# Performance work log

Measured on AMD Instinct MI355X. Metric: run time of the kernel, lower is better.

The kernel has to match this reference:

```python
import jax, jax.numpy as jnp
import numpy as np

L = 4      # number of Verifier layers in the linked list
D = 1536   # constraint matrix dimension


def setup_inputs() -> dict:
    key = jax.random.key(0)
    ks = jax.random.split(key, 6)
    scale = 0.02  # keep chained matmul magnitudes sane
    lb = jax.random.normal(ks[0], (1, D), jnp.float32)
    ub = lb + jax.random.uniform(ks[1], (1, D), jnp.float32)  # ensure lb <= ub
    lcs = scale * jax.random.normal(ks[2], (L, D, D), jnp.float32)
    ucs = lcs + scale * jax.random.uniform(ks[3], (L, D, D), jnp.float32)
    lc_bias = jax.random.normal(ks[4], (L, D), jnp.float32)
    uc_bias = lc_bias + jax.random.uniform(ks[5], (L, D), jnp.float32)
    return {"lb": lb, "ub": ub, "lcs": lcs, "ucs": ucs,
            "lc_bias": lc_bias, "uc_bias": uc_bias}


def reference(lb, ub, lcs, ucs, lc_bias, uc_bias):
    pos = lambda x: jnp.maximum(x, 0.0)
    neg = lambda x: jnp.minimum(x, 0.0)
    n_layers = lcs.shape[0]

    # Layer 0 forward: its backsubstitution returns these bounds unchanged
    # (prev is None), and all later backsubs terminate on these stored bounds.
    lb0 = lb @ pos(lcs[0]).T + ub @ neg(lcs[0]).T + lc_bias[0]
    ub0 = ub @ pos(ucs[0]).T + lb @ neg(ucs[0]).T + uc_bias[0]
    cur_lb, cur_ub = lb0, ub0

    for k in range(1, n_layers):
        # backsubstitution from layer k: start with transposed constraint
        C_lc, C_uc = lcs[k].T, ucs[k].T           # [D, D]
        C_lcb, C_ucb = lc_bias[k], uc_bias[k]     # [D]
        # recurse through layers k-1 .. 0, combining constraints
        for j in range(k - 1, -1, -1):
            pU, nU = pos(C_uc), neg(C_uc)
            pL, nL = pos(C_lc), neg(C_lc)
            new_ucb = uc_bias[j] @ pU + lc_bias[j] @ nU + C_ucb
            new_uc = ucs[j].T @ pU + lcs[j].T @ nU
            new_lcb = lc_bias[j] @ pL + uc_bias[j] @ nL + C_lcb
            new_lc = lcs[j].T @ pL + ucs[j].T @ nL
            C_lc, C_uc, C_lcb, C_ucb = new_lc, new_uc, new_lcb, new_ucb
        # apply combined constraint to layer-0 stored bounds
        cur_lb = lb0 @ pos(C_lc) + ub0 @ neg(C_lc) + C_lcb
        cur_ub = ub0 @ pos(C_uc) + lb0 @ neg(C_uc) + C_ucb

    return cur_lb, cur_ub
```

## Files before the change

### kernel.cpp

```cpp
#include <hip/hip_runtime.h>

#define D 1536
#define BT 96
#define BK 64
#define NT (D / BK)
#define TT 64
#define TILE_E (BT * BK)
#define BUF_E (3 * TILE_E)

typedef unsigned short u16;
typedef short bf16x8 __attribute__((ext_vector_type(8)));
typedef float f32x4 __attribute__((ext_vector_type(4)));

static __device__ __forceinline__ u16 f2bf(float f) {
    unsigned u; __builtin_memcpy(&u, &f, 4);
    unsigned r = (u + 0x7FFFu + ((u >> 16) & 1u)) >> 16;
    return (u16)r;
}
static __device__ __forceinline__ float bf2f(u16 s) {
    unsigned u = ((unsigned)s) << 16;
    float f; __builtin_memcpy(&f, &u, 4); return f;
}

#define GLDS(g, s) __builtin_amdgcn_global_load_lds( \
    (const __attribute__((address_space(1))) void*)(g), \
    (__attribute__((address_space(3))) void*)(s), 16, 0, 0)

#define MFMA16(a, b, c) __builtin_amdgcn_mfma_f32_16x16x32_bf16(a, b, c, 0, 0, 0)

__global__ __launch_bounds__(256) void prep_k(
    const float* __restrict__ lcs, const float* __restrict__ ucs,
    u16* __restrict__ BsT, u16* __restrict__ BdT,
    u16* __restrict__ Ga, u16* __restrict__ Gc)
{
    const int z = blockIdx.z;
    const int r0 = blockIdx.y * TT, c0 = blockIdx.x * TT;
    const int tid = threadIdx.x;

    if (z == 3) {
#pragma unroll
        for (int m = 0; m < 2; ++m) {
            const float* src = (m ? lcs : ucs) + (size_t)3 * D * D;
            u16* dst = m ? Gc : Ga;
#pragma unroll
            for (int i = 0; i < 2; ++i) {
                int r = (tid >> 3) + i * 32, cc = (tid & 7) * 8;
                const float* p = src + (size_t)(r0 + r) * D + c0 + cc;
                f32x4 x0 = *(const f32x4*)p;
                f32x4 x1 = *(const f32x4*)(p + 4);
                bf16x8 y;
#pragma unroll
                for (int e = 0; e < 4; ++e) { y[e] = (short)f2bf(x0[e]); y[e + 4] = (short)f2bf(x1[e]); }
                *(bf16x8*)(dst + (size_t)(r0 + r) * D + c0 + cc) = y;
            }
        }
        return;
    }

    __shared__ u16 ts[TT][TT + 8];
    __shared__ u16 td[TT][TT + 8];
    const float* srcl = lcs + (size_t)z * D * D;
    const float* srcu = ucs + (size_t)z * D * D;
#pragma unroll
    for (int i = 0; i < 2; ++i) {
        int c = tid + i * 256; int r = c >> 3, v = c & 7;
        size_t off = (size_t)(r0 + r) * D + c0 + v * 8;
        f32x4 l0 = *(const f32x4*)(srcl + off);
        f32x4 l1 = *(const f32x4*)(srcl + off + 4);
        f32x4 u0 = *(const f32x4*)(srcu + off);
        f32x4 u1 = *(const f32x4*)(srcu + off + 4);
        bf16x8 ys, yd;
#pragma unroll
        for (int e = 0; e < 4; ++e) {
            ys[e]     = (short)f2bf((u0[e] + l0[e]) * 0.5f);
            yd[e]     = (short)f2bf((u0[e] - l0[e]) * 0.5f);
            ys[e + 4] = (short)f2bf((u1[e] + l1[e]) * 0.5f);
            yd[e + 4] = (short)f2bf((u1[e] - l1[e]) * 0.5f);
        }
        *(bf16x8*)&ts[r][v * 8] = ys;
        *(bf16x8*)&td[r][v * 8] = yd;
    }
    __syncthreads();
#pragma unroll
    for (int i = 0; i < 2; ++i) {
        int c = tid + i * 256; int rr = c >> 3, v = c & 7;
        bf16x8 xs, xd;
#pragma unroll
        for (int e = 0; e < 8; ++e) { xs[e] = (short)ts[v * 8 + e][rr]; xd[e] = (short)td[v * 8 + e][rr]; }
        size_t off = (size_t)z * D * D + (size_t)(c0 + rr) * D + r0 + v * 8;
        *(bf16x8*)(BsT + off) = xs;
        *(bf16x8*)(BdT + off) = xd;
    }
}

__global__ __launch_bounds__(256) void vec_k(
    const float* __restrict__ lb, const float* __restrict__ ub,
    const float* __restrict__ lcs, const float* __restrict__ ucs,
    const float* __restrict__ lcb, const float* __restrict__ ucb,
    float* __restrict__ lb0, float* __restrict__ ub0,
    float* __restrict__ cb_uc, float* __restrict__ cb_lc)
{
    const int tt = blockIdx.x * 4 + (threadIdx.x >> 6);
    const int lane = threadIdx.x & 63;
    const int which = tt / D;
    const int row_n = tt - which * D;

    const float* row; const float* vp; const float* vn;
    if (which == 0)      { row = lcs + (size_t)row_n * D;               vp = lb;           vn = ub; }
    else if (which == 1) { row = ucs + (size_t)row_n * D;               vp = ub;           vn = lb; }
    else if (which == 2) { row = ucs + (size_t)(3 * (size_t)D * D) + (size_t)row_n * D; vp = ucb + 2 * D; vn = lcb + 2 * D; }
    else                 { row = lcs + (size_t)(3 * (size_t)D * D) + (size_t)row_n * D; vp = lcb + 2 * D; vn = ucb + 2 * D; }

    float s = 0.f;
    for (int c2 = 0; c2 < D / 256; ++c2) {
        int base = (c2 * 64 + lane) * 4;
        f32x4 g = *(const f32x4*)(row + base);
        f32x4 p = *(const f32x4*)(vp + base);
        f32x4 m = *(const f32x4*)(vn + base);
#pragma unroll
        for (int e = 0; e < 4; ++e) s += g[e] * (g[e] > 0.f ? p[e] : m[e]);
    }
#pragma unroll
    for (int o = 32; o; o >>= 1) s += __shfl_down(s, o);
    if (lane == 0) {
        if (which == 0)      lb0[row_n] = s + lcb[row_n];
        else if (which == 1) ub0[row_n] = s + ucb[row_n];
        else if (which == 2) cb_uc[row_n] = s + ucb[3 * D + row_n];
        else                 cb_lc[row_n] = s + lcb[3 * D + row_n];
    }
}

__global__ __launch_bounds__(256, 2) void gemm_step(
    const u16* __restrict__ Guc, const u16* __restrict__ Glc,
    const u16* __restrict__ Bs, const u16* __restrict__ Bd,
    u16* __restrict__ outU, u16* __restrict__ outL,
    const float* __restrict__ ucbN, const float* __restrict__ lcbN,
    float* __restrict__ cb_uc, float* __restrict__ cb_lc)
{
    __shared__ u16 smem[2 * BUF_E];
    const int wg  = blockIdx.x + 16 * blockIdx.y + 256 * blockIdx.z;
    const int xcd = wg & 7, idx = wg >> 3;
    const int chain = xcd >> 2;
    const int bx = (xcd & 1) * 8 + (idx & 7);
    const int by = ((xcd >> 1) & 1) * 8 + (idx >> 3);

    const u16* A = chain ? Glc : Guc;
    u16* out = chain ? outL : outU;
    const unsigned sgn = chain ? 0x80008000u : 0u;
    const int r0 = by * BT, c0 = bx * BT;
    const int tid = threadIdx.x, lane = tid & 63, wid = tid >> 6;
    const int mb = (wid >> 1) * 48, nb = (wid & 1) * 48;
    const int lrow = lane & 15, lk = lane >> 4;

    f32x4 acc[3][3] = {};

#define STAGE(kt, sbuf) do { \
    _Pragma("unroll") for (int i_ = 0; i_ < 9; ++i_) { \
        const int idx_ = (i_ % 3) * 256 + tid; \
        const int row_ = idx_ >> 3; \
        const int kcg_ = (tid & 7) ^ (row_ & 7); \
        const u16* base_ = (i_ < 3) ? (A + (size_t)(r0 + row_) * D) \
                        : ((i_ < 6) ? (Bs + (size_t)(c0 + row_) * D) \
                                    : (Bd + (size_t)(c0 + row_) * D)); \
        GLDS(base_ + (kt) + kcg_ * 8, (char*)(sbuf) + (i_ * 256 + wid * 64) * 16); \
    } } while (0)

    int offA[3], offBs[3], offBd[3];
#pragma unroll
    for (int mi = 0; mi < 3; ++mi) {
        int row = mb + mi * 16 + lrow;
        offA[mi] = row * BK + (lk ^ (row & 7)) * 8;
    }
#pragma unroll
    for (int ni = 0; ni < 3; ++ni) {
        int row = nb + ni * 16 + lrow;
        offBs[ni] = TILE_E + row * BK;
        offBd[ni] = 2 * TILE_E + row * BK;
    }

    STAGE(0, smem);
    STAGE(BK, smem + BUF_E);

#pragma unroll 1
    for (int t = 0; t < NT; ++t) {
        if (t < NT - 1) { asm volatile("s_waitcnt vmcnt(9)" ::: "memory"); }
        else            { asm volatile("s_waitcnt vmcnt(0)" ::: "memory"); }
        __builtin_amdgcn_sched_barrier(0);
        __builtin_amdgcn_s_barrier();

        const u16* sb = smem + (t & 1) * BUF_E;
#pragma unroll
        for (int ks = 0; ks < 2; ++ks) {
            const int slot = ks * 4;
            bf16x8 a[3], x[3];
#pragma unroll
            for (int mi = 0; mi < 3; ++mi) {
                int row = mb + mi * 16 + lrow;
                a[mi] = *(const bf16x8*)(sb + row * BK + ((slot + lk) ^ (row & 7)) * 8);
                union { bf16x8 v; unsigned u[4]; } ti, to;
                ti.v = a[mi];
#pragma unroll
                for (int q = 0; q < 4; ++q) to.u[q] = (ti.u[q] & 0x7FFF7FFFu) ^ sgn;
                x[mi] = to.v;
            }
#pragma unroll
            for (int ni = 0; ni < 3; ++ni) {
                int row = nb + ni * 16 + lrow;
                int o = row * BK + ((slot + lk) ^ (row & 7)) * 8;
                bf16x8 bs = *(const bf16x8*)(sb + TILE_E + o);
                bf16x8 bd = *(const bf16x8*)(sb + 2 * TILE_E + o);
#pragma unroll
                for (int mi = 0; mi < 3; ++mi) {
                    acc[mi][ni] = MFMA16(a[mi], bs, acc[mi][ni]);
                    acc[mi][ni] = MFMA16(x[mi], bd, acc[mi][ni]);
                }
            }
        }
        __builtin_amdgcn_s_barrier();
        if (t + 2 < NT)
            STAGE((t + 2) * BK, smem + (t & 1) * BUF_E);
    }

    if (ucbN) {
        const float* pb_ = chain ? lcbN : ucbN;
        const float* nb_ = chain ? ucbN : lcbN;
        float* cb = chain ? cb_lc : cb_uc;
        float pbv[3], nbv[3];
#pragma unroll
        for (int ni = 0; ni < 3; ++ni) {
            int c = c0 + nb + ni * 16 + lrow;
            pbv[ni] = pb_[c]; nbv[ni] = nb_[c];
        }
#pragma unroll
        for (int mi = 0; mi < 3; ++mi)
#pragma unroll
            for (int q = 0; q < 4; ++q) {
                float s = 0.f;
#pragma unroll
                for (int ni = 0; ni < 3; ++ni) {
                    float g = acc[mi][ni][q];
                    s += g * (g > 0.f ? pbv[ni] : nbv[ni]);
                }
                s += __shfl_xor(s, 1); s += __shfl_xor(s, 2);
                s += __shfl_xor(s, 4); s += __shfl_xor(s, 8);
                if (lrow == 0)
                    atomicAdd(&cb[r0 + mb + mi * 16 + lk * 4 + q], s);
            }
    }

#pragma unroll
    for (int mi = 0; mi < 3; ++mi)
#pragma unroll
        for (int ni = 0; ni < 3; ++ni) {
            int c = c0 + nb + ni * 16 + lrow;
            int rbase = r0 + mb + mi * 16 + lk * 4;
#pragma unroll
            for (int q = 0; q < 4; ++q)
                out[(size_t)(rbase + q) * D + c] = f2bf(acc[mi][ni][q]);
        }
#undef STAGE
}

__global__ __launch_bounds__(256) void final_k(
    const u16* __restrict__ Guc, const u16* __restrict__ Glc,
    const float* __restrict__ cb_uc, const float* __restrict__ cb_lc,
    const float* __restrict__ lb0, const float* __restrict__ ub0,
    float* __restrict__ out)
{
    const int gw = blockIdx.x * 4 + (threadIdx.x >> 6);
    const int lane = threadIdx.x & 63;
    const int which = gw >= D;
    const int n = which ? gw - D : gw;
    const u16* row = (which ? Guc : Glc) + (size_t)n * D;
    const float* vp = which ? ub0 : lb0;
    const float* vn = which ? lb0 : ub0;
    float s = 0.f;
    for (int c2 = 0; c2 < D / 512; ++c2) {
        int base = (c2 * 64 + lane) * 8;
        bf16x8 g8 = *(const bf16x8*)(row + base);
        f32x4 p0 = *(const f32x4*)(vp + base);
        f32x4 p1 = *(const f32x4*)(vp + base + 4);
        f32x4 n0 = *(const f32x4*)(vn + base);
        f32x4 n1 = *(const f32x4*)(vn + base + 4);
#pragma unroll
        for (int e = 0; e < 8; ++e) {
            float g = bf2f((u16)g8[e]);
            float pv = e < 4 ? p0[e] : p1[e - 4];
            float nv = e < 4 ? n0[e] : n1[e - 4];
            s += g * (g > 0.f ? pv : nv);
        }
    }
#pragma unroll
    for (int o = 32; o; o >>= 1) s += __shfl_down(s, o);
    if (lane == 0) {
        float b = (which ? cb_uc : cb_lc)[n];
        out[which * D + n] = s + b;
    }
}

extern "C" void kernel_launch(void* const* d_in, const int* in_sizes, int n_in,
                              void* d_out, int out_size, void* d_ws, size_t ws_size,
                              hipStream_t stream) {
    const float* lb  = (const float*)d_in[0];
    const float* ub  = (const float*)d_in[1];
    const float* lcs = (const float*)d_in[2];
    const float* ucs = (const float*)d_in[3];
    const float* lcb = (const float*)d_in[4];
    const float* ucb = (const float*)d_in[5];
    float* out = (float*)d_out;

    const size_t DD = (size_t)D * D;
    u16* ws   = (u16*)d_ws;
    u16* BsT = ws;
    u16* BdT = BsT + 3 * DD;
    u16* Ga = BdT + 3 * DD;
    u16* Gb = Ga + DD;
    u16* Gc = Gb + DD;
    u16* Gd = Gc + DD;
    float* fbuf  = (float*)(Gd + DD);
    float* lb0   = fbuf;
    float* ub0   = fbuf + D;
    float* cb_uc = fbuf + 2 * D;
    float* cb_lc = fbuf + 3 * D;

    prep_k<<<dim3(D / TT, D / TT, 4), 256, 0, stream>>>(lcs, ucs, BsT, BdT, Ga, Gc);
    vec_k<<<dim3(4 * D / 4), 256, 0, stream>>>(lb, ub, lcs, ucs, lcb, ucb, lb0, ub0, cb_uc, cb_lc);

    u16* curU = Ga; u16* curL = Gc;
    u16* altU = Gb; u16* altL = Gd;
    for (int j = 2; j >= 0; --j) {
        const float* ucbN = (j > 0) ? (ucb + (size_t)(j - 1) * D) : nullptr;
        const float* lcbN = (j > 0) ? (lcb + (size_t)(j - 1) * D) : nullptr;
        gemm_step<<<dim3(16, 16, 2), 256, 0, stream>>>(
            curU, curL, BsT + (size_t)j * DD, BdT + (size_t)j * DD, altU, altL,
            ucbN, lcbN, cb_uc, cb_lc);
        u16* t;
        t = curU; curU = altU; altU = t;
        t = curL; curL = altL; altL = t;
    }
    final_k<<<dim3(2 * D / 4), 256, 0, stream>>>(curU, curL, cb_uc, cb_lc, lb0, ub0, out);
}
```

Baseline: 129.1 us.

## Use per-wave private LDS staging to drop workgroup barriers in GEMM step

The shared 96x64 double-buffered tile, loaded cooperatively and guarded by two workgroup barriers per k-step, is replaced with per-wave private buffers. Each wave loads only the 48 rows of A, Bs and Bd it consumes, using BK=32 and a new XOR swizzle. The next stage's loads are issued right after the fragments are read into registers, and the MFMA block runs at raised priority. This removes all s_barrier synchronisation, but each operand row is now loaded by two waves, which doubles global and LDS traffic, and the number of k-iterations doubles.

```diff
diff --git a/kernel.cpp b/kernel.cpp
--- a/kernel.cpp
+++ b/kernel.cpp
@@ -2,11 +2,10 @@
 
 #define D 1536
 #define BT 96
-#define BK 64
-#define NT (D / BK)
+#define BKW 32
+#define NTW (D / BKW)
 #define TT 64
-#define TILE_E (BT * BK)
-#define BUF_E (3 * TILE_E)
+#define PBUF_B 9216
 
 typedef unsigned short u16;
 typedef short bf16x8 __attribute__((ext_vector_type(8)));
@@ -137,7 +136,7 @@
     const float* __restrict__ ucbN, const float* __restrict__ lcbN,
     float* __restrict__ cb_uc, float* __restrict__ cb_lc)
 {
-    __shared__ u16 smem[2 * BUF_E];
+    __shared__ u16 smem[4 * 2 * PBUF_B / 2];
     const int wg  = blockIdx.x + 16 * blockIdx.y + 256 * blockIdx.z;
     const int xcd = wg & 7, idx = wg >> 3;
     const int chain = xcd >> 2;
@@ -152,74 +151,74 @@
     const int mb = (wid >> 1) * 48, nb = (wid & 1) * 48;
     const int lrow = lane & 15, lk = lane >> 4;
 
+    const int srow = lane >> 2;
+    const int kslot = (lane & 3) ^ ((lane >> 3) & 3);
+    const u16* gsrc[9];
+#pragma unroll
+    for (int j = 0; j < 3; ++j) {
+        gsrc[j]     = A  + (size_t)(r0 + mb + j * 16 + srow) * D + kslot * 8;
+        gsrc[3 + j] = Bs + (size_t)(c0 + nb + j * 16 + srow) * D + kslot * 8;
+        gsrc[6 + j] = Bd + (size_t)(c0 + nb + j * 16 + srow) * D + kslot * 8;
+    }
+    char* wbase = (char*)smem + wid * (2 * PBUF_B);
+
+#define STAGEW(t) do { \
+    char* db_ = wbase + ((t) & 1) * PBUF_B; \
+    _Pragma("unroll") for (int c_ = 0; c_ < 9; ++c_) \
+        GLDS(gsrc[c_] + (size_t)(t) * BKW, db_ + c_ * 1024); \
+    } while (0)
+
+    const int pso = (lk ^ ((lrow >> 1) & 3)) * 8;
+    int offA[3], offBs[3], offBd[3];
+#pragma unroll
+    for (int mi = 0; mi < 3; ++mi) offA[mi] = (mi * 16 + lrow) * BKW + pso;
+#pragma unroll
+    for (int ni = 0; ni < 3; ++ni) {
+        offBs[ni] = 1536 + (ni * 16 + lrow) * BKW + pso;
+        offBd[ni] = 3072 + (ni * 16 + lrow) * BKW + pso;
+    }
+
     f32x4 acc[3][3] = {};
 
-#define STAGE(kt, sbuf) do { \
-    _Pragma("unroll") for (int i_ = 0; i_ < 9; ++i_) { \
-        const int idx_ = (i_ % 3) * 256 + tid; \
-        const int row_ = idx_ >> 3; \
-        const int kcg_ = (tid & 7) ^ (row_ & 7); \
-        const u16* base_ = (i_ < 3) ? (A + (size_t)(r0 + row_) * D) \
-                        : ((i_ < 6) ? (Bs + (size_t)(c0 + row_) * D) \
-                                    : (Bd + (size_t)(c0 + row_) * D)); \
-        GLDS(base_ + (kt) + kcg_ * 8, (char*)(sbuf) + (i_ * 256 + wid * 64) * 16); \
-    } } while (0)
-
-    int offA[3], offBs[3], offBd[3];
-#pragma unroll
-    for (int mi = 0; mi < 3; ++mi) {
-        int row = mb + mi * 16 + lrow;
-        offA[mi] = row * BK + (lk ^ (row & 7)) * 8;
-    }
-#pragma unroll
-    for (int ni = 0; ni < 3; ++ni) {
-        int row = nb + ni * 16 + lrow;
-        offBs[ni] = TILE_E + row * BK;
-        offBd[ni] = 2 * TILE_E + row * BK;
-    }
-
-    STAGE(0, smem);
-    STAGE(BK, smem + BUF_E);
-
-#pragma unroll 1
-    for (int t = 0; t < NT; ++t) {
-        if (t < NT - 1) { asm volatile("s_waitcnt vmcnt(9)" ::: "memory"); }
-        else            { asm volatile("s_waitcnt vmcnt(0)" ::: "memory"); }
+    STAGEW(0);
+    STAGEW(1);
+
+#pragma unroll 2
+    for (int t = 0; t < NTW; ++t) {
+        if (t < NTW - 1) { asm volatile("s_waitcnt vmcnt(9)" ::: "memory"); }
+        else             { asm volatile("s_waitcnt vmcnt(0)" ::: "memory"); }
         __builtin_amdgcn_sched_barrier(0);
-        __builtin_amdgcn_s_barrier();
-
-        const u16* sb = smem + (t & 1) * BUF_E;
-#pragma unroll
-        for (int ks = 0; ks < 2; ++ks) {
-            const int slot = ks * 4;
-            bf16x8 a[3], x[3];
+
+        const u16* sb = (const u16*)(wbase + (t & 1) * PBUF_B);
+        bf16x8 a[3], x[3], bsv[3], bdv[3];
+#pragma unroll
+        for (int mi = 0; mi < 3; ++mi) {
+            a[mi] = *(const bf16x8*)(sb + offA[mi]);
+            union { bf16x8 v; unsigned u[4]; } ti, to;
+            ti.v = a[mi];
+#pragma unroll
+            for (int q = 0; q < 4; ++q) to.u[q] = (ti.u[q] & 0x7FFF7FFFu) ^ sgn;
+            x[mi] = to.v;
+        }
+#pragma unroll
+        for (int ni = 0; ni < 3; ++ni) {
+            bsv[ni] = *(const bf16x8*)(sb + offBs[ni]);
+            bdv[ni] = *(const bf16x8*)(sb + offBd[ni]);
+        }
+        __builtin_amdgcn_sched_barrier(0);
+        if (t + 2 < NTW) STAGEW(t + 2);
+
+        __builtin_amdgcn_s_setprio(1);
+#pragma unroll
+        for (int ni = 0; ni < 3; ++ni)
 #pragma unroll
             for (int mi = 0; mi < 3; ++mi) {
-                int row = mb + mi * 16 + lrow;
-                a[mi] = *(const bf16x8*)(sb + row * BK + ((slot + lk) ^ (row & 7)) * 8);
-                union { bf16x8 v; unsigned u[4]; } ti, to;
-                ti.v = a[mi];
-#pragma unroll
-                for (int q = 0; q < 4; ++q) to.u[q] = (ti.u[q] & 0x7FFF7FFFu) ^ sgn;
-                x[mi] = to.v;
+                acc[mi][ni] = MFMA16(a[mi], bsv[ni], acc[mi][ni]);
+                acc[mi][ni] = MFMA16(x[mi], bdv[ni], acc[mi][ni]);
             }
-#pragma unroll
-            for (int ni = 0; ni < 3; ++ni) {
-                int row = nb + ni * 16 + lrow;
-                int o = row * BK + ((slot + lk) ^ (row & 7)) * 8;
-                bf16x8 bs = *(const bf16x8*)(sb + TILE_E + o);
-                bf16x8 bd = *(const bf16x8*)(sb + 2 * TILE_E + o);
-#pragma unroll
-                for (int mi = 0; mi < 3; ++mi) {
-                    acc[mi][ni] = MFMA16(a[mi], bs, acc[mi][ni]);
-                    acc[mi][ni] = MFMA16(x[mi], bd, acc[mi][ni]);
-                }
-            }
-        }
-        __builtin_amdgcn_s_barrier();
-        if (t + 2 < NT)
-            STAGE((t + 2) * BK, smem + (t & 1) * BUF_E);
-    }
+        __builtin_amdgcn_s_setprio(0);
+    }
+#undef STAGEW
 
     if (ucbN) {
         const float* pb_ = chain ? lcbN : ucbN;
@@ -258,7 +257,6 @@
             for (int q = 0; q < 4; ++q)
                 out[(size_t)(rbase + q) * D + c] = f2bf(acc[mi][ni][q]);
         }
-#undef STAGE
 }
 
 __global__ __launch_bounds__(256) void final_k(
```

Measured after the change: 184.8 us. +43.1%, slower.

## Switch GEMM step to triple-buffered BK=32 pipeline with single barrier per tile

Applied to the files above, without the earlier changes.

Halves the K tile to 32, moves from two to three LDS buffers, and unrolls the main loop by three so each iteration reads its operands into registers, issues the next prefetch before the MFMAs, and needs only one barrier instead of two. Global-to-LDS source addresses are precomputed once per thread, the swizzle changes to a 4-way XOR, and MFMA issue is wrapped in s_setprio. The aim is better overlap of loads with matrix math and less per-iteration address and sync overhead, at the cost of more loop iterations, uneven per-thread load counts (tid<128 handles a fifth chunk) and more LDS, which may affect occupancy at 2 blocks per CU.

```diff
diff --git a/kernel.cpp b/kernel.cpp
--- a/kernel.cpp
+++ b/kernel.cpp
@@ -2,11 +2,10 @@
 
 #define D 1536
 #define BT 96
-#define BK 64
-#define NT (D / BK)
+#define BK 32
+#define NTW (D / BK)
 #define TT 64
-#define TILE_E (BT * BK)
-#define BUF_E (3 * TILE_E)
+#define BUF_E 9216
 
 typedef unsigned short u16;
 typedef short bf16x8 __attribute__((ext_vector_type(8)));
@@ -137,7 +136,7 @@
     const float* __restrict__ ucbN, const float* __restrict__ lcbN,
     float* __restrict__ cb_uc, float* __restrict__ cb_lc)
 {
-    __shared__ u16 smem[2 * BUF_E];
+    __shared__ u16 smem[3 * BUF_E];
     const int wg  = blockIdx.x + 16 * blockIdx.y + 256 * blockIdx.z;
     const int xcd = wg & 7, idx = wg >> 3;
     const int chain = xcd >> 2;
@@ -146,80 +145,85 @@
 
     const u16* A = chain ? Glc : Guc;
     u16* out = chain ? outL : outU;
-    const unsigned sgn = chain ? 0x80008000u : 0u;
+    const unsigned amask = chain ? 0xFFFFFFFFu : 0x7FFF7FFFu;
+    const unsigned omask = chain ? 0x80008000u : 0u;
     const int r0 = by * BT, c0 = bx * BT;
     const int tid = threadIdx.x, lane = tid & 63, wid = tid >> 6;
     const int mb = (wid >> 1) * 48, nb = (wid & 1) * 48;
     const int lrow = lane & 15, lk = lane >> 4;
+    const int ok5 = (tid < 128);
+
+    const u16* gsrc[5];
+#pragma unroll
+    for (int i = 0; i < 5; ++i) {
+        int c = tid + i * 256; if (c >= 1152) c = 1151;
+        int b = c / 384, ix = c - b * 384;
+        int row = ix >> 2, kc = ix & 3;
+        int kcg = kc ^ (row & 3);
+        gsrc[i] = ((b == 0) ? A + (size_t)(r0 + row) * D
+                 : (b == 1) ? Bs + (size_t)(c0 + row) * D
+                            : Bd + (size_t)(c0 + row) * D) + kcg * 8;
+    }
+
+#define STAGE(kt, sbuf) do { \
+    _Pragma("unroll") for (int i_ = 0; i_ < 5; ++i_) \
+        if (i_ < 4 || ok5) \
+            GLDS(gsrc[i_] + (kt), (char*)(sbuf) + (i_ * 256 + wid * 64) * 16); \
+    } while (0)
+
+    const int pso = (lk ^ (lrow & 3)) * 8;
+    int offA[3], offBs[3], offBd[3];
+#pragma unroll
+    for (int mi = 0; mi < 3; ++mi) offA[mi] = (mb + mi * 16 + lrow) * BK + pso;
+#pragma unroll
+    for (int ni = 0; ni < 3; ++ni) {
+        int o = (nb + ni * 16 + lrow) * BK + pso;
+        offBs[ni] = 3072 + o;
+        offBd[ni] = 6144 + o;
+    }
 
     f32x4 acc[3][3] = {};
-
-#define STAGE(kt, sbuf) do { \
-    _Pragma("unroll") for (int i_ = 0; i_ < 9; ++i_) { \
-        const int idx_ = (i_ % 3) * 256 + tid; \
-        const int row_ = idx_ >> 3; \
-        const int kcg_ = (tid & 7) ^ (row_ & 7); \
-        const u16* base_ = (i_ < 3) ? (A + (size_t)(r0 + row_) * D) \
-                        : ((i_ < 6) ? (Bs + (size_t)(c0 + row_) * D) \
-                                    : (Bd + (size_t)(c0 + row_) * D)); \
-        GLDS(base_ + (kt) + kcg_ * 8, (char*)(sbuf) + (i_ * 256 + wid * 64) * 16); \
-    } } while (0)
-
-    int offA[3], offBs[3], offBd[3];
-#pragma unroll
-    for (int mi = 0; mi < 3; ++mi) {
-        int row = mb + mi * 16 + lrow;
-        offA[mi] = row * BK + (lk ^ (row & 7)) * 8;
-    }
-#pragma unroll
-    for (int ni = 0; ni < 3; ++ni) {
-        int row = nb + ni * 16 + lrow;
-        offBs[ni] = TILE_E + row * BK;
-        offBd[ni] = 2 * TILE_E + row * BK;
-    }
 
     STAGE(0, smem);
     STAGE(BK, smem + BUF_E);
 
+#define ONE_ITER(t, RB, SB) do { \
+    if ((t) < NTW - 1) { \
+        if (ok5) { asm volatile("s_waitcnt vmcnt(5)" ::: "memory"); } \
+        else     { asm volatile("s_waitcnt vmcnt(4)" ::: "memory"); } \
+    } else       { asm volatile("s_waitcnt vmcnt(0)" ::: "memory"); } \
+    __builtin_amdgcn_sched_barrier(0); \
+    __builtin_amdgcn_s_barrier(); \
+    const u16* sb_ = smem + (RB) * BUF_E; \
+    bf16x8 a_[3], bs_[3], bd_[3], x_[3]; \
+    _Pragma("unroll") for (int mi_ = 0; mi_ < 3; ++mi_) \
+        a_[mi_] = *(const bf16x8*)(sb_ + offA[mi_]); \
+    _Pragma("unroll") for (int ni_ = 0; ni_ < 3; ++ni_) { \
+        bs_[ni_] = *(const bf16x8*)(sb_ + offBs[ni_]); \
+        bd_[ni_] = *(const bf16x8*)(sb_ + offBd[ni_]); } \
+    if ((t) + 2 < NTW) STAGE(((t) + 2) * BK, smem + (SB) * BUF_E); \
+    _Pragma("unroll") for (int mi_ = 0; mi_ < 3; ++mi_) { \
+        union { bf16x8 v; unsigned u[4]; } ti_, to_; \
+        ti_.v = a_[mi_]; \
+        _Pragma("unroll") for (int q_ = 0; q_ < 4; ++q_) \
+            to_.u[q_] = (ti_.u[q_] & amask) | omask; \
+        x_[mi_] = to_.v; } \
+    __builtin_amdgcn_s_setprio(1); \
+    _Pragma("unroll") for (int ni_ = 0; ni_ < 3; ++ni_) \
+    _Pragma("unroll") for (int mi_ = 0; mi_ < 3; ++mi_) { \
+        acc[mi_][ni_] = MFMA16(a_[mi_], bs_[ni_], acc[mi_][ni_]); \
+        acc[mi_][ni_] = MFMA16(x_[mi_], bd_[ni_], acc[mi_][ni_]); } \
+    __builtin_amdgcn_s_setprio(0); \
+    } while (0)
+
 #pragma unroll 1
-    for (int t = 0; t < NT; ++t) {
-        if (t < NT - 1) { asm volatile("s_waitcnt vmcnt(9)" ::: "memory"); }
-        else            { asm volatile("s_waitcnt vmcnt(0)" ::: "memory"); }
-        __builtin_amdgcn_sched_barrier(0);
-        __builtin_amdgcn_s_barrier();
-
-        const u16* sb = smem + (t & 1) * BUF_E;
-#pragma unroll
-        for (int ks = 0; ks < 2; ++ks) {
-            const int slot = ks * 4;
-            bf16x8 a[3], x[3];
-#pragma unroll
-            for (int mi = 0; mi < 3; ++mi) {
-                int row = mb + mi * 16 + lrow;
-                a[mi] = *(const bf16x8*)(sb + row * BK + ((slot + lk) ^ (row & 7)) * 8);
-                union { bf16x8 v; unsigned u[4]; } ti, to;
-                ti.v = a[mi];
-#pragma unroll
-                for (int q = 0; q < 4; ++q) to.u[q] = (ti.u[q] & 0x7FFF7FFFu) ^ sgn;
-                x[mi] = to.v;
-            }
-#pragma unroll
-            for (int ni = 0; ni < 3; ++ni) {
-                int row = nb + ni * 16 + lrow;
-                int o = row * BK + ((slot + lk) ^ (row & 7)) * 8;
-                bf16x8 bs = *(const bf16x8*)(sb + TILE_E + o);
-                bf16x8 bd = *(const bf16x8*)(sb + 2 * TILE_E + o);
-#pragma unroll
-                for (int mi = 0; mi < 3; ++mi) {
-                    acc[mi][ni] = MFMA16(a[mi], bs, acc[mi][ni]);
-                    acc[mi][ni] = MFMA16(x[mi], bd, acc[mi][ni]);
-                }
-            }
-        }
-        __builtin_amdgcn_s_barrier();
-        if (t + 2 < NT)
-            STAGE((t + 2) * BK, smem + (t & 1) * BUF_E);
-    }
+    for (int tb = 0; tb < NTW; tb += 3) {
+        ONE_ITER(tb,     0, 2);
+        ONE_ITER(tb + 1, 1, 0);
+        ONE_ITER(tb + 2, 2, 1);
+    }
+#undef ONE_ITER
+#undef STAGE
 
     if (ucbN) {
         const float* pb_ = chain ? lcbN : ucbN;
@@ -258,7 +262,6 @@
             for (int q = 0; q < 4; ++q)
                 out[(size_t)(rbase + q) * D + c] = f2bf(acc[mi][ni][q]);
         }
-#undef STAGE
 }
 
 __global__ __launch_bounds__(256) void final_k(
```

Measured after the change: 146.5 us. +13.4%, slower.
